# Kernel tuning notes

Measured on AMD Instinct MI355X. Metric: run time of the kernel, lower is better.

## Reference

```python
import jax, jax.numpy as jnp
import numpy as np

B, LQ, LP, H = 16, 2048, 2048, 1024

def setup_inputs() -> dict:
    key = jax.random.key(0)
    kq, kp, kw = jax.random.split(key, 3)
    q = jax.random.normal(kq, (B, LQ, H), dtype=jnp.float32)
    p = jax.random.normal(kp, (B, LP, H), dtype=jnp.float32)
    W = jax.random.normal(kw, (H, H), dtype=jnp.float32) * (1.0 / np.sqrt(H))
    b = jnp.zeros((H,), dtype=jnp.float32)
    return {"q": q, "p": p, "W": W, "b": b}

def reference(q, p, W, b):
    # shared linear + ReLU projections (torch Linear: x @ W.T + b)
    q_lin = jax.nn.relu(jnp.einsum('bqh,oh->bqo', q, W) + b)  # [B,LQ,H]
    p_lin = jax.nn.relu(jnp.einsum('bph,oh->bpo', p, W) + b)  # [B,LP,H]
    # unscaled cross-attention scores: p_lin @ q_lin^T -> [B,LP,LQ]
    scores = jnp.einsum('bpd,bqd->bpq', p_lin, q_lin)
    att = jax.nn.softmax(scores, axis=2)
    # context-aware query: att @ q_lin -> [B,LP,H]
    return jnp.einsum('bpq,bqd->bpd', att, q_lin)
```

## Files before the change

### kernel.cpp

```cpp
#include <hip/hip_runtime.h>


#define LQN 2048
#define LPN 2048
#define HD  1024
#define NBATCH 16

typedef _Float16 half8 __attribute__((ext_vector_type(8)));
typedef _Float16 half4_t __attribute__((ext_vector_type(4)));
typedef float f32x4 __attribute__((ext_vector_type(4)));

#define GLP(src, dst) __builtin_amdgcn_global_load_lds(                          \
    (const __attribute__((address_space(1))) void*)(src),                        \
    (__attribute__((address_space(3))) void*)(dst), 16, 0, 0)

__global__ __launch_bounds__(256) void cvt_f32_f16(const float* __restrict__ in,
                                                   _Float16* __restrict__ out,
                                                   long n4) {
  long i0 = (long)blockIdx.x * blockDim.x + threadIdx.x;
  long stride = (long)gridDim.x * blockDim.x;
  for (long i = i0; i < n4; i += stride) {
    float4 v = ((const float4*)in)[i];
    half4_t h = {(_Float16)v.x, (_Float16)v.y, (_Float16)v.z, (_Float16)v.w};
    ((half4_t*)out)[i] = h;
  }
}


#define SYNC_PRE                                        \
  __builtin_amdgcn_sched_barrier(0);                    \
  __builtin_amdgcn_s_barrier();                         \
  asm volatile("s_waitcnt lgkmcnt(0)" ::: "memory");    \
  __builtin_amdgcn_sched_barrier(0);                    \
  __builtin_amdgcn_s_setprio(1);

#define SYNC_POST                                       \
  __builtin_amdgcn_s_setprio(0);                        \
  __builtin_amdgcn_sched_barrier(0);                    \
  __builtin_amdgcn_s_barrier();

#define SYNC_POST_VM                                    \
  __builtin_amdgcn_s_setprio(0);                        \
  __builtin_amdgcn_sched_barrier(0);                    \
  asm volatile("s_waitcnt vmcnt(4)" ::: "memory");      \
  __builtin_amdgcn_s_barrier();

#define LOADA(qm, buf)                                                            \
  _Pragma("unroll")                                                               \
  for (int mi = 0; mi < 4; ++mi) {                                                \
    areg[mi][0] = *(const half8*)(smA + (buf)*32768 + abase + ((qm)*4+mi)*4096);  \
    areg[mi][1] = *(const half8*)(smA + (buf)*32768 + abase + ((qm)*4+mi)*4096 + 64); \
  }

#define LOADB(qn, buf)                                                            \
  _Pragma("unroll")                                                               \
  for (int ni = 0; ni < 2; ++ni) {                                                \
    breg[ni][0] = *(const half8*)(smB + (buf)*32768 + bbase + ((qn)*2+ni)*8192);  \
    breg[ni][1] = *(const half8*)(smB + (buf)*32768 + bbase + ((qn)*2+ni)*8192 + 64); \
  }

#define STAGEA(t, h, buf) do {                                                    \
  GLP(gA + (size_t)((h)*128)*lda + (size_t)(t)*64,                                \
      smW + (buf)*32768 + (h)*16384 + wid*1024);                                  \
  GLP(gA + (size_t)((h)*128+64)*lda + (size_t)(t)*64,                             \
      smW + (buf)*32768 + (h)*16384 + 8192 + wid*1024);                           \
} while (0)

#define STAGEB(t, h, buf) do {                                                    \
  GLP(gB + (size_t)((h)*128)*ldb + (size_t)(t)*64,                                \
      smW + 65536 + (buf)*32768 + (h)*16384 + wid*1024);                          \
  GLP(gB + (size_t)((h)*128+64)*ldb + (size_t)(t)*64,                             \
      smW + 65536 + (buf)*32768 + (h)*16384 + 8192 + wid*1024);                   \
} while (0)

#define DO_MFMA(qm, qn)                                                           \
  _Pragma("unroll")                                                               \
  for (int mi = 0; mi < 4; ++mi) {                                                \
    _Pragma("unroll")                                                             \
    for (int ni = 0; ni < 2; ++ni) {                                              \
      acc[(qm)*4+mi][(qn)*2+ni] = __builtin_amdgcn_mfma_f32_16x16x32_f16(         \
          areg[mi][0], breg[ni][0], acc[(qm)*4+mi][(qn)*2+ni], 0, 0, 0);          \
      acc[(qm)*4+mi][(qn)*2+ni] = __builtin_amdgcn_mfma_f32_16x16x32_f16(         \
          areg[mi][1], breg[ni][1], acc[(qm)*4+mi][(qn)*2+ni], 0, 0, 0);          \
    }                                                                             \
  }

template <int EPI>
__global__ __launch_bounds__(512, 2) void gemm8p(
    const _Float16* __restrict__ A, const _Float16* __restrict__ B,
    const float* __restrict__ bias, void* __restrict__ Cv,
    _Float16* __restrict__ CT, int K, int lda, int ldb, int ldc,
    long sAz, long sBz, long sCz) {
  extern __shared__ __align__(16) char smem[];
  const char* smA = smem;
  const char* smB = smem + 65536;
  char* smW = smem;

  const int tid = threadIdx.x;
  const int lane = tid & 63, wid = tid >> 6;
  const int l16 = lane & 15, lhi = lane >> 4;
  const int wr = wid >> 2, wcn = wid & 3;

  const int lswz = ((l16 >> 2) & 1) << 5;
  const int abase = (wr * 2048 + l16 * 128 + lhi * 16) ^ lswz;
  const int bbase = (wcn * 2048 + l16 * 128 + lhi * 16) ^ lswz;

  const int tl = tid ^ (((tid >> 5) & 1) << 1);
  const int srow = tl >> 3;
  const int scol = (tl & 7) * 8;

  const int bm0 = blockIdx.x * 256, bn0 = blockIdx.y * 256;
  const _Float16* gA = A + (size_t)blockIdx.z * sAz + (size_t)(bm0 + srow) * lda + scol;
  const _Float16* gB = B + (size_t)blockIdx.z * sBz + (size_t)(bn0 + srow) * ldb + scol;

  const int NT = K >> 6, NI = K >> 7;

  f32x4 acc[8][4] = {};
  half8 areg[4][2], breg[2][2];

  STAGEA(0, 0, 0); STAGEB(0, 0, 0);
  STAGEA(0, 1, 0); STAGEB(0, 1, 0);
  STAGEA(1, 0, 1); STAGEB(1, 0, 1);
  __builtin_amdgcn_sched_barrier(0);
  asm volatile("s_waitcnt vmcnt(4)" ::: "memory");
  __builtin_amdgcn_s_barrier();

  for (int i = 0; i < NI; ++i) {
    const int t1 = 2 * i + 1;
    int t2 = 2 * i + 2; if (t2 > NT - 1) t2 = NT - 1;
    int t3 = 2 * i + 3; if (t3 > NT - 1) t3 = NT - 1;
    LOADA(0, 0) LOADB(0, 0) STAGEA(t1, 1, 1);
    SYNC_PRE DO_MFMA(0, 0) SYNC_POST
    LOADB(1, 0) STAGEB(t1, 1, 1);
    SYNC_PRE DO_MFMA(0, 1) SYNC_POST
    LOADA(1, 0) LOADB(0, 0) STAGEA(t2, 0, 0);
    SYNC_PRE DO_MFMA(1, 0) SYNC_POST
    LOADB(1, 0) STAGEB(t2, 0, 0);
    SYNC_PRE DO_MFMA(1, 1) SYNC_POST_VM
    LOADA(0, 1) LOADB(0, 1) STAGEA(t2, 1, 0);
    SYNC_PRE DO_MFMA(0, 0) SYNC_POST
    LOADB(1, 1) STAGEB(t2, 1, 0);
    SYNC_PRE DO_MFMA(0, 1) SYNC_POST
    LOADA(1, 1) LOADB(0, 1) STAGEA(t3, 0, 1);
    SYNC_PRE DO_MFMA(1, 0) SYNC_POST
    LOADB(1, 1) STAGEB(t3, 0, 1);
    SYNC_PRE DO_MFMA(1, 1) SYNC_POST_VM
  }

  if constexpr (EPI == 0) {
    float* Cb = (float*)Cv + (size_t)blockIdx.z * sCz;
#pragma unroll
    for (int m = 0; m < 8; ++m) {
      int row0 = bm0 + m * 32 + wr * 16 + lhi * 4;
#pragma unroll
      for (int n = 0; n < 4; ++n) {
        int col = bn0 + n * 64 + wcn * 16 + l16;
#pragma unroll
        for (int v = 0; v < 4; ++v)
          Cb[(size_t)(row0 + v) * ldc + col] = acc[m][n][v];
      }
    }
  } else {
    _Float16* Cb = (_Float16*)Cv;
#pragma unroll
    for (int n = 0; n < 4; ++n) {
      int col = bn0 + n * 64 + wcn * 16 + l16;
      float bv = bias[col];
#pragma unroll
      for (int m = 0; m < 8; ++m) {
        int row0 = bm0 + m * 32 + wr * 16 + lhi * 4;
        float v0 = fmaxf(acc[m][n][0] + bv, 0.f);
        float v1 = fmaxf(acc[m][n][1] + bv, 0.f);
        float v2 = fmaxf(acc[m][n][2] + bv, 0.f);
        float v3 = fmaxf(acc[m][n][3] + bv, 0.f);
        Cb[(size_t)(row0 + 0) * ldc + col] = (_Float16)v0;
        Cb[(size_t)(row0 + 1) * ldc + col] = (_Float16)v1;
        Cb[(size_t)(row0 + 2) * ldc + col] = (_Float16)v2;
        Cb[(size_t)(row0 + 3) * ldc + col] = (_Float16)v3;
        if constexpr (EPI == 1) {
          half4_t h = {(_Float16)v0, (_Float16)v1, (_Float16)v2, (_Float16)v3};
          int bz = row0 >> 11, qi = row0 & 2047;
          *(half4_t*)&CT[(size_t)bz * ((size_t)HD * LQN) + (size_t)col * LQN + qi] = h;
        }
      }
    }
  }
}

__global__ __launch_bounds__(256) void softmax_k(float* __restrict__ buf) {
  __shared__ float red[4];
  const int t = threadIdx.x;
  float* s = buf + (size_t)blockIdx.x * 2048;
  float4 v0 = ((const float4*)s)[t * 2];
  float4 v1 = ((const float4*)s)[t * 2 + 1];
  float m = fmaxf(fmaxf(fmaxf(v0.x, v0.y), fmaxf(v0.z, v0.w)),
                  fmaxf(fmaxf(v1.x, v1.y), fmaxf(v1.z, v1.w)));
#pragma unroll
  for (int o = 32; o; o >>= 1) m = fmaxf(m, __shfl_xor(m, o));
  if ((t & 63) == 0) red[t >> 6] = m;
  __syncthreads();
  m = fmaxf(fmaxf(red[0], red[1]), fmaxf(red[2], red[3]));
  float e[8];
  e[0] = __expf(v0.x - m); e[1] = __expf(v0.y - m);
  e[2] = __expf(v0.z - m); e[3] = __expf(v0.w - m);
  e[4] = __expf(v1.x - m); e[5] = __expf(v1.y - m);
  e[6] = __expf(v1.z - m); e[7] = __expf(v1.w - m);
  float sum = ((e[0] + e[1]) + (e[2] + e[3])) + ((e[4] + e[5]) + (e[6] + e[7]));
#pragma unroll
  for (int o = 32; o; o >>= 1) sum += __shfl_xor(sum, o);
  __syncthreads();
  if ((t & 63) == 0) red[t >> 6] = sum;
  __syncthreads();
  sum = (red[0] + red[1]) + (red[2] + red[3]);
  float inv = 1.f / sum;
  half8 h;
  h[0] = (_Float16)(e[0] * inv); h[1] = (_Float16)(e[1] * inv);
  h[2] = (_Float16)(e[2] * inv); h[3] = (_Float16)(e[3] * inv);
  h[4] = (_Float16)(e[4] * inv); h[5] = (_Float16)(e[5] * inv);
  h[6] = (_Float16)(e[6] * inv); h[7] = (_Float16)(e[7] * inv);
  ((half8*)s)[t] = h;
}

extern "C" void kernel_launch(void* const* d_in, const int* in_sizes, int n_in,
                              void* d_out, int out_size, void* d_ws, size_t ws_size,
                              hipStream_t stream) {
  const float* q = (const float*)d_in[0];
  const float* p = (const float*)d_in[1];
  const float* W = (const float*)d_in[2];
  const float* bias = (const float*)d_in[3];
  float* out = (float*)d_out;
  char* ws = (char*)d_ws;

  _Float16* qf    = (_Float16*)(ws);
  _Float16* pf    = (_Float16*)(ws + 67108864L);
  _Float16* qlin  = (_Float16*)(ws + 134217728L);
  _Float16* plin  = (_Float16*)(ws + 201326592L);
  _Float16* qlinT = (_Float16*)(ws + 268435456L);
  _Float16* Wf    = (_Float16*)(ws + 335544320L);
  float* scores   = (float*)ws;

  const long nQ = (long)NBATCH * LQN * HD;
  const size_t SH = 131072;

  cvt_f32_f16<<<2048, 256, 0, stream>>>(q, qf, nQ / 4);
  cvt_f32_f16<<<2048, 256, 0, stream>>>(p, pf, nQ / 4);
  cvt_f32_f16<<<64, 256, 0, stream>>>(W, Wf, (long)HD * HD / 4);

  gemm8p<1><<<dim3(NBATCH * LQN / 256, HD / 256, 1), 512, SH, stream>>>(
      qf, Wf, bias, qlin, qlinT, HD, HD, HD, HD, 0, 0, 0);
  gemm8p<2><<<dim3(NBATCH * LPN / 256, HD / 256, 1), 512, SH, stream>>>(
      pf, Wf, bias, plin, (_Float16*)0, HD, HD, HD, HD, 0, 0, 0);

  for (int c = 0; c < 2; ++c) {
    int bz0 = c * 8;
    gemm8p<0><<<dim3(LPN / 256, LQN / 256, 8), 512, SH, stream>>>(
        plin + (size_t)bz0 * LPN * HD, qlin + (size_t)bz0 * LQN * HD,
        (const float*)0, scores, (_Float16*)0,
        HD, HD, HD, LQN,
        (long)LPN * HD, (long)LQN * HD, (long)LPN * LQN);
    softmax_k<<<8 * LPN, 256, 0, stream>>>(scores);
    gemm8p<0><<<dim3(LPN / 256, HD / 256, 8), 512, SH, stream>>>(
        (const _Float16*)scores, qlinT + (size_t)bz0 * HD * LQN,
        (const float*)0, out + (size_t)bz0 * LPN * HD, (_Float16*)0,
        LQN, 2 * LQN, LQN, HD,
        (long)LPN * 2 * LQN, (long)HD * LQN, (long)LPN * HD);
  }
}
```

Measured before the change: 638.7 us.

## Use XOR LDS swizzle, reuse B fragments, and merge q/p projection GEMMs

Replaces the LDS swizzle with a full 8-way XOR pattern on both the staging writes and the fragment reads, to cut bank conflicts. B fragments are now kept in registers across the qm halves, so redundant LDS reads are dropped at the cost of more VGPRs. The q and p projection GEMMs become a single launch over twice as many rows, relying on pf sitting directly after qf and plin directly after qlin in the workspace. Only row blocks from the q half write the transposed output.

Result: faster. 581.5 us (-9.0%).

```diff
diff --git a/kernel.cpp b/kernel.cpp
--- a/kernel.cpp
+++ b/kernel.cpp
@@ -48,15 +48,15 @@
 #define LOADA(qm, buf)                                                            \
   _Pragma("unroll")                                                               \
   for (int mi = 0; mi < 4; ++mi) {                                                \
-    areg[mi][0] = *(const half8*)(smA + (buf)*32768 + abase + ((qm)*4+mi)*4096);  \
-    areg[mi][1] = *(const half8*)(smA + (buf)*32768 + abase + ((qm)*4+mi)*4096 + 64); \
+    areg[mi][0] = *(const half8*)(smA + (buf)*32768 + a0 + ((qm)*4+mi)*4096);     \
+    areg[mi][1] = *(const half8*)(smA + (buf)*32768 + a1 + ((qm)*4+mi)*4096);     \
   }
 
 #define LOADB(qn, buf)                                                            \
   _Pragma("unroll")                                                               \
   for (int ni = 0; ni < 2; ++ni) {                                                \
-    breg[ni][0] = *(const half8*)(smB + (buf)*32768 + bbase + ((qn)*2+ni)*8192);  \
-    breg[ni][1] = *(const half8*)(smB + (buf)*32768 + bbase + ((qn)*2+ni)*8192 + 64); \
+    bregs[qn][ni][0] = *(const half8*)(smB + (buf)*32768 + b0 + ((qn)*2+ni)*8192);\
+    bregs[qn][ni][1] = *(const half8*)(smB + (buf)*32768 + b1 + ((qn)*2+ni)*8192);\
   }
 
 #define STAGEA(t, h, buf) do {                                                    \
@@ -79,9 +79,9 @@
     _Pragma("unroll")                                                             \
     for (int ni = 0; ni < 2; ++ni) {                                              \
       acc[(qm)*4+mi][(qn)*2+ni] = __builtin_amdgcn_mfma_f32_16x16x32_f16(         \
-          areg[mi][0], breg[ni][0], acc[(qm)*4+mi][(qn)*2+ni], 0, 0, 0);          \
+          areg[mi][0], bregs[qn][ni][0], acc[(qm)*4+mi][(qn)*2+ni], 0, 0, 0);     \
       acc[(qm)*4+mi][(qn)*2+ni] = __builtin_amdgcn_mfma_f32_16x16x32_f16(         \
-          areg[mi][1], breg[ni][1], acc[(qm)*4+mi][(qn)*2+ni], 0, 0, 0);          \
+          areg[mi][1], bregs[qn][ni][1], acc[(qm)*4+mi][(qn)*2+ni], 0, 0, 0);     \
     }                                                                             \
   }
 
@@ -101,13 +101,14 @@
   const int l16 = lane & 15, lhi = lane >> 4;
   const int wr = wid >> 2, wcn = wid & 3;
 
-  const int lswz = ((l16 >> 2) & 1) << 5;
-  const int abase = (wr * 2048 + l16 * 128 + lhi * 16) ^ lswz;
-  const int bbase = (wcn * 2048 + l16 * 128 + lhi * 16) ^ lswz;
-
-  const int tl = tid ^ (((tid >> 5) & 1) << 1);
-  const int srow = tl >> 3;
-  const int scol = (tl & 7) * 8;
+  const int mask = (l16 & 7) << 4;
+  const int a0 = (wr * 2048 + l16 * 128 + lhi * 16) ^ mask;
+  const int a1 = a0 ^ 64;
+  const int b0 = (wcn * 2048 + l16 * 128 + lhi * 16) ^ mask;
+  const int b1 = b0 ^ 64;
+
+  const int srow = tid >> 3;
+  const int scol = (((tid & 7) ^ ((tid >> 3) & 7)) << 3);
 
   const int bm0 = blockIdx.x * 256, bn0 = blockIdx.y * 256;
   const _Float16* gA = A + (size_t)blockIdx.z * sAz + (size_t)(bm0 + srow) * lda + scol;
@@ -116,7 +117,7 @@
   const int NT = K >> 6, NI = K >> 7;
 
   f32x4 acc[8][4] = {};
-  half8 areg[4][2], breg[2][2];
+  half8 areg[4][2], bregs[2][2][2];
 
   STAGEA(0, 0, 0); STAGEB(0, 0, 0);
   STAGEA(0, 1, 0); STAGEB(0, 1, 0);
@@ -133,17 +134,17 @@
     SYNC_PRE DO_MFMA(0, 0) SYNC_POST
     LOADB(1, 0) STAGEB(t1, 1, 1);
     SYNC_PRE DO_MFMA(0, 1) SYNC_POST
-    LOADA(1, 0) LOADB(0, 0) STAGEA(t2, 0, 0);
+    LOADA(1, 0) STAGEA(t2, 0, 0);
     SYNC_PRE DO_MFMA(1, 0) SYNC_POST
-    LOADB(1, 0) STAGEB(t2, 0, 0);
+    STAGEB(t2, 0, 0);
     SYNC_PRE DO_MFMA(1, 1) SYNC_POST_VM
     LOADA(0, 1) LOADB(0, 1) STAGEA(t2, 1, 0);
     SYNC_PRE DO_MFMA(0, 0) SYNC_POST
     LOADB(1, 1) STAGEB(t2, 1, 0);
     SYNC_PRE DO_MFMA(0, 1) SYNC_POST
-    LOADA(1, 1) LOADB(0, 1) STAGEA(t3, 0, 1);
+    LOADA(1, 1) STAGEA(t3, 0, 1);
     SYNC_PRE DO_MFMA(1, 0) SYNC_POST
-    LOADB(1, 1) STAGEB(t3, 0, 1);
+    STAGEB(t3, 0, 1);
     SYNC_PRE DO_MFMA(1, 1) SYNC_POST_VM
   }
 
@@ -162,6 +163,7 @@
     }
   } else {
     _Float16* Cb = (_Float16*)Cv;
+    const bool doCT = (bm0 < NBATCH * LQN);
 #pragma unroll
     for (int n = 0; n < 4; ++n) {
       int col = bn0 + n * 64 + wcn * 16 + l16;
@@ -177,7 +179,7 @@
         Cb[(size_t)(row0 + 1) * ldc + col] = (_Float16)v1;
         Cb[(size_t)(row0 + 2) * ldc + col] = (_Float16)v2;
         Cb[(size_t)(row0 + 3) * ldc + col] = (_Float16)v3;
-        if constexpr (EPI == 1) {
+        if (doCT) {
           half4_t h = {(_Float16)v0, (_Float16)v1, (_Float16)v2, (_Float16)v3};
           int bz = row0 >> 11, qi = row0 & 2047;
           *(half4_t*)&CT[(size_t)bz * ((size_t)HD * LQN) + (size_t)col * LQN + qi] = h;
@@ -246,10 +248,8 @@
   cvt_f32_f16<<<2048, 256, 0, stream>>>(p, pf, nQ / 4);
   cvt_f32_f16<<<64, 256, 0, stream>>>(W, Wf, (long)HD * HD / 4);
 
-  gemm8p<1><<<dim3(NBATCH * LQN / 256, HD / 256, 1), 512, SH, stream>>>(
+  gemm8p<1><<<dim3(2 * NBATCH * LQN / 256, HD / 256, 1), 512, SH, stream>>>(
       qf, Wf, bias, qlin, qlinT, HD, HD, HD, HD, 0, 0, 0);
-  gemm8p<2><<<dim3(NBATCH * LPN / 256, HD / 256, 1), 512, SH, stream>>>(
-      pf, Wf, bias, plin, (_Float16*)0, HD, HD, HD, HD, 0, 0, 0);
 
   for (int c = 0; c < 2; ++c) {
     int bz0 = c * 8;
```
